# Kernel optimization log

Hardware: AMD Instinct MI355X
Metric: run time of the kernel (lower is better)

## Reference

```python
import jax, jax.numpy as jnp
import numpy as np

N_NODES = 10000
N_EDGES = 160000
BN_EPS = 1e-5


def _sage(xx, src, dst, Wl, bl, Wr, n):
    # SAGEConv: lin_l(mean of in-neighbors) + lin_r(x)
    s = jax.ops.segment_sum(xx[src], dst, num_segments=n)
    cnt = jax.ops.segment_sum(jnp.ones((src.shape[0], 1), xx.dtype), dst, num_segments=n)
    mean = s / jnp.maximum(cnt, 1.0)
    return mean @ Wl + bl + xx @ Wr


def _gin(xx, src, dst, W1, b1, W2, b2, n):
    # GINConv (eps=0): MLP(x + sum of neighbors), MLP = Lin-ReLU-Lin-ReLU
    agg = xx + jax.ops.segment_sum(xx[src], dst, num_segments=n)
    h = jax.nn.relu(agg @ W1 + b1)
    return jax.nn.relu(h @ W2 + b2)


def _gat(xx, s2, d2, W, a_s, a_d, b, heads, ch, n):
    # GATConv with self-loops already appended in (s2, d2)
    h = (xx @ W).reshape(n, heads, ch)          # [N,H,C]
    al_s = (h * a_s).sum(-1)                     # [N,H]
    al_d = (h * a_d).sum(-1)                     # [N,H]
    e = jax.nn.leaky_relu(al_s[s2] + al_d[d2], negative_slope=0.2)  # [E',H]
    m = jax.ops.segment_max(e, d2, num_segments=n)
    ex = jnp.exp(e - m[d2])
    den = jax.ops.segment_sum(ex, d2, num_segments=n)
    coef = ex / den[d2]                          # segment softmax over dst
    out = jax.ops.segment_sum(h[s2] * coef[:, :, None], d2, num_segments=n)
    return out.reshape(n, heads * ch) + b


def reference(x, edge_index, train_edge_id,
              Wp1, bp1, Wp2, bp2, Wp3, bp3,
              sage1_Wl, sage1_bl, sage1_Wr, sage2_Wl, sage2_bl, sage2_Wr,
              gin1_W1, gin1_b1, gin1_W2, gin1_b2,
              gin2_W1, gin2_b1, gin2_W2, gin2_b2, gin_lin_W, gin_lin_b,
              gat1_W, gat1_as, gat1_ad, gat1_b,
              gat2_W, gat2_as, gat2_ad, gat2_b,
              fusion_w, lin1_W, lin1_b, lin2_W, lin2_b, fc2_W, fc2_b):
    n = x.shape[0]
    src, dst = edge_index[0], edge_index[1]
    # --- ppc: PointNet-style encoder: per-point MLP (16->64->128->256) + max pool over points ---
    pts = x[:, :, :16]                            # [N,L,16]
    h = jax.nn.relu(pts @ Wp1 + bp1)
    h = jax.nn.relu(h @ Wp2 + bp2)
    h = jax.nn.relu(h @ Wp3 + bp3)
    feat = h.max(axis=1)                          # [N,256]
    # --- SAGE branch ---
    hs = jax.nn.relu(_sage(feat, src, dst, sage1_Wl, sage1_bl, sage1_Wr, n))
    out_sage = _sage(hs, src, dst, sage2_Wl, sage2_bl, sage2_Wr, n)
    # --- GIN branch ---
    hg = jax.nn.relu(_gin(feat, src, dst, gin1_W1, gin1_b1, gin1_W2, gin1_b2, n))
    hg = jax.nn.relu(_gin(hg, src, dst, gin2_W1, gin2_b1, gin2_W2, gin2_b2, n))
    out_gin = hg @ gin_lin_W + gin_lin_b
    # --- GAT branch (self-loops per PyG default) ---
    loop = jnp.arange(n)
    s2 = jnp.concatenate([src, loop])
    d2 = jnp.concatenate([dst, loop])
    ha = jax.nn.relu(_gat(feat, s2, d2, gat1_W, gat1_as, gat1_ad, gat1_b, 8, 10, n))
    out_gat = _gat(ha, s2, d2, gat2_W, gat2_as, gat2_ad, gat2_b, 1, 512, n)
    # --- weighted fusion + batch norm (batch stats, no affine) ---
    y = fusion_w[0] * out_sage + fusion_w[1] * out_gin + fusion_w[2] * out_gat
    mu = y.mean(axis=0)
    var = y.var(axis=0)
    y = (y - mu) / jnp.sqrt(var + BN_EPS)
    # --- head ---
    y = jax.nn.relu(y @ lin1_W + lin1_b)
    y = y @ lin2_W + lin2_b
    # --- edge-pair gather + multiply for link scoring ---
    nid = edge_index[:, train_edge_id]            # [2,T]
    z = y[nid[0]] * y[nid[1]]
    return z @ fc2_W + fc2_b                      # [T,7]


def setup_inputs() -> dict:
    key = jax.random.key(0)
    ks = iter(jax.random.split(key, 64))
    def nrm(shape, s=0.02):
        return jax.random.normal(next(ks), shape, dtype=jnp.float32) * s
    inp = {}
    inp['x'] = jax.random.normal(next(ks), (N_NODES, 128, 16), dtype=jnp.float32)
    inp['edge_index'] = jax.random.randint(next(ks), (2, N_EDGES), 0, N_NODES, dtype=jnp.int32)
    inp['train_edge_id'] = jax.random.randint(next(ks), (50000,), 0, N_EDGES, dtype=jnp.int32)
    # ppc point encoder
    inp['Wp1'] = nrm((16, 64)); inp['bp1'] = nrm((64,))
    inp['Wp2'] = nrm((64, 128)); inp['bp2'] = nrm((128,))
    inp['Wp3'] = nrm((128, 256)); inp['bp3'] = nrm((256,))
    # SAGE: 256->128->512
    inp['sage1_Wl'] = nrm((256, 128)); inp['sage1_bl'] = nrm((128,)); inp['sage1_Wr'] = nrm((256, 128))
    inp['sage2_Wl'] = nrm((128, 512)); inp['sage2_bl'] = nrm((512,)); inp['sage2_Wr'] = nrm((128, 512))
    # GIN: 2 convs (256->128->128, 128->128->128) + lin 128->512
    inp['gin1_W1'] = nrm((256, 128)); inp['gin1_b1'] = nrm((128,))
    inp['gin1_W2'] = nrm((128, 128)); inp['gin1_b2'] = nrm((128,))
    inp['gin2_W1'] = nrm((128, 128)); inp['gin2_b1'] = nrm((128,))
    inp['gin2_W2'] = nrm((128, 128)); inp['gin2_b2'] = nrm((128,))
    inp['gin_lin_W'] = nrm((128, 512)); inp['gin_lin_b'] = nrm((512,))
    # GAT: layer1 256 -> 8 heads x 10 (concat=80), layer2 80 -> 512 (1 head)
    inp['gat1_W'] = nrm((256, 80)); inp['gat1_as'] = nrm((8, 10)); inp['gat1_ad'] = nrm((8, 10)); inp['gat1_b'] = nrm((80,))
    inp['gat2_W'] = nrm((80, 512)); inp['gat2_as'] = nrm((1, 512)); inp['gat2_ad'] = nrm((1, 512)); inp['gat2_b'] = nrm((512,))
    # fusion + head
    inp['fusion_w'] = jnp.ones((3,), jnp.float32)
    inp['lin1_W'] = nrm((512, 512)); inp['lin1_b'] = nrm((512,))
    inp['lin2_W'] = nrm((512, 512)); inp['lin2_b'] = nrm((512,))
    inp['fc2_W'] = nrm((512, 7)); inp['fc2_b'] = nrm((7,))
    return inp
```

## Files before the change

kernel.cpp:

```cpp
#include <hip/hip_runtime.h>
#include <math.h>

#define NN 10000
#define NE 160000
#define NT 50000

typedef unsigned short u16;
typedef unsigned int u32;
typedef __attribute__((ext_vector_type(8))) short bf16x8;
typedef __attribute__((ext_vector_type(4))) float f32x4;

__device__ __forceinline__ float bf2f(u16 u) { return __uint_as_float(((u32)u) << 16); }
__device__ __forceinline__ u16 f2bf(float f) {
    u32 x = __float_as_uint(f);
    return (u16)((x + 0x7fffu + ((x >> 16) & 1u)) >> 16);
}
__device__ __forceinline__ u32 cvtpk(float a, float b) {
    u32 r;
    asm("v_cvt_pk_bf16_f32 %0, %1, %2" : "=v"(r) : "v"(a), "v"(b));
    return r;
}
__device__ __forceinline__ float lrelu(float x) { return x > 0.f ? x : 0.2f * x; }

#define MFMA16(a, b, c) __builtin_amdgcn_mfma_f32_16x16x32_bf16((a), (b), (c), 0, 0, 0)

__global__ void k_cvt_x(const float* __restrict__ x, u32* __restrict__ xb) {
    const int total = NN * 128 * 8;
    for (int i = blockIdx.x * 256 + threadIdx.x; i < total; i += gridDim.x * 256) {
        float2 v = ((const float2*)x)[i];
        xb[i] = cvtpk(v.x, v.y);
    }
}

__global__ void k_wfrag(const float* __restrict__ W1, const float* __restrict__ W2,
                        const float* __restrict__ W3,
                        u16* __restrict__ W1f, u16* __restrict__ W2f, u16* __restrict__ W3f) {
    int i = blockIdx.x * 256 + threadIdx.x;
    if (i < 2048) {
        int e = i & 7, l = (i >> 3) & 63, nt = i >> 9;
        int k = (l >> 4) * 8 + e, c = nt * 16 + (l & 15);
        W1f[i] = (k < 16) ? f2bf(W1[k * 64 + c]) : (u16)0;
    }
    if (i < 8192) {
        int e = i & 7, l = (i >> 3) & 63, nt = (i >> 9) & 7, ks = i >> 12;
        int k = ks * 32 + (l >> 4) * 8 + e, c = nt * 16 + (l & 15);
        W2f[i] = f2bf(W2[k * 128 + c]);
    }
    if (i < 32768) {
        int e = i & 7, l = (i >> 3) & 63, nt = (i >> 9) & 15, ks = i >> 13;
        int k = ks * 32 + (l >> 4) * 8 + e, c = nt * 16 + (l & 15);
        W3f[i] = f2bf(W3[k * 256 + c]);
    }
}

__global__ void k_pack(const float* __restrict__ W, u16* __restrict__ Wf, int K, int Mt) {
    int total = (((K + 63) & ~63) >> 5) * Mt * 512;
    for (int i = blockIdx.x * 256 + threadIdx.x; i < total; i += gridDim.x * 256) {
        int e = i & 7, l = (i >> 3) & 63, mt = (i >> 9) % Mt, kk = i / (Mt << 9);
        int k = (kk << 5) + ((l >> 4) << 3) + e;
        int c = (mt << 4) + (l & 15);
        Wf[i] = (k < K) ? f2bf(W[(size_t)k * (Mt << 4) + c]) : (u16)0;
    }
}

__global__ __launch_bounds__(256) void k_pointnet_mfma(
    const u16* __restrict__ xb,
    const u16* __restrict__ W1f, const float* __restrict__ b1,
    const u16* __restrict__ W2f, const float* __restrict__ b2,
    const u16* __restrict__ W3f, const float* __restrict__ b3,
    u16* __restrict__ featb)
{
    __shared__ u16 buf[16384];

    const int node = blockIdx.x;
    const int t = threadIdx.x;
    const int w = t >> 6;
    const int l = t & 63;
    const int lr = l & 15;
    const int lg = l >> 4;

    {
        bf16x8 a0 = {0,0,0,0,0,0,0,0}, a1 = a0;
        if (lg < 2) {
            const u16* px = xb + ((size_t)node * 128 + w * 32 + lr) * 16 + lg * 8;
            a0 = *(const bf16x8*)px;
            a1 = *(const bf16x8*)(px + 256);
        }
        f32x4 acc[2][4];
        #pragma unroll
        for (int nt = 0; nt < 4; ++nt) {
            float bv = b1[nt * 16 + lr];
            f32x4 ci = {bv, bv, bv, bv};
            bf16x8 bf_ = *(const bf16x8*)(W1f + (nt * 64 + l) * 8);
            acc[0][nt] = MFMA16(a0, bf_, ci);
            acc[1][nt] = MFMA16(a1, bf_, ci);
        }
        #pragma unroll
        for (int mt = 0; mt < 2; ++mt) {
            #pragma unroll
            for (int nt = 0; nt < 4; ++nt) {
                int col = nt * 16 + lr;
                int r0 = w * 32 + mt * 16 + lg * 4;
                u32 p01 = cvtpk(fmaxf(acc[mt][nt][0], 0.f), fmaxf(acc[mt][nt][1], 0.f));
                u32 p23 = cvtpk(fmaxf(acc[mt][nt][2], 0.f), fmaxf(acc[mt][nt][3], 0.f));
                buf[((r0    ) * 64 + col) ^ (((r0    ) & 7) << 3)] = (u16)p01;
                buf[((r0 + 1) * 64 + col) ^ (((r0 + 1) & 7) << 3)] = (u16)(p01 >> 16);
                buf[((r0 + 2) * 64 + col) ^ (((r0 + 2) & 7) << 3)] = (u16)p23;
                buf[((r0 + 3) * 64 + col) ^ (((r0 + 3) & 7) << 3)] = (u16)(p23 >> 16);
            }
        }
    }

    {
        bf16x8 af[2][2];
        #pragma unroll
        for (int mt = 0; mt < 2; ++mt) {
            #pragma unroll
            for (int ks = 0; ks < 2; ++ks) {
                int row = w * 32 + mt * 16 + lr;
                int elem = row * 64 + ks * 32 + lg * 8;
                af[mt][ks] = *(const bf16x8*)&buf[elem ^ ((row & 7) << 3)];
            }
        }
        __syncthreads();

        f32x4 acc2[2][8];
        #pragma unroll
        for (int nt = 0; nt < 8; ++nt) {
            float bv = b2[nt * 16 + lr];
            f32x4 ci = {bv, bv, bv, bv};
            acc2[0][nt] = ci;
            acc2[1][nt] = ci;
        }
        #pragma unroll
        for (int ks = 0; ks < 2; ++ks) {
            #pragma unroll
            for (int nt = 0; nt < 8; ++nt) {
                bf16x8 bf_ = *(const bf16x8*)(W2f + ((ks * 8 + nt) * 64 + l) * 8);
                acc2[0][nt] = MFMA16(af[0][ks], bf_, acc2[0][nt]);
                acc2[1][nt] = MFMA16(af[1][ks], bf_, acc2[1][nt]);
            }
        }
        #pragma unroll
        for (int mt = 0; mt < 2; ++mt) {
            #pragma unroll
            for (int nt = 0; nt < 8; ++nt) {
                int col = nt * 16 + lr;
                int r0 = w * 32 + mt * 16 + lg * 4;
                u32 p01 = cvtpk(fmaxf(acc2[mt][nt][0], 0.f), fmaxf(acc2[mt][nt][1], 0.f));
                u32 p23 = cvtpk(fmaxf(acc2[mt][nt][2], 0.f), fmaxf(acc2[mt][nt][3], 0.f));
                buf[((r0    ) * 128 + col) ^ (((r0    ) & 7) << 3)] = (u16)p01;
                buf[((r0 + 1) * 128 + col) ^ (((r0 + 1) & 7) << 3)] = (u16)(p01 >> 16);
                buf[((r0 + 2) * 128 + col) ^ (((r0 + 2) & 7) << 3)] = (u16)p23;
                buf[((r0 + 3) * 128 + col) ^ (((r0 + 3) & 7) << 3)] = (u16)(p23 >> 16);
            }
        }
    }
    __syncthreads();

    {
        float pmax[4] = {0.f, 0.f, 0.f, 0.f};
        #pragma unroll
        for (int half = 0; half < 2; ++half) {
            f32x4 acc3[4][4];
            #pragma unroll
            for (int nt = 0; nt < 4; ++nt) {
                float bv = b3[w * 64 + nt * 16 + lr];
                f32x4 ci = {bv, bv, bv, bv};
                #pragma unroll
                for (int mt = 0; mt < 4; ++mt) acc3[mt][nt] = ci;
            }
            #pragma unroll
            for (int ks = 0; ks < 4; ++ks) {
                bf16x8 bf_[4];
                #pragma unroll
                for (int nt = 0; nt < 4; ++nt)
                    bf_[nt] = *(const bf16x8*)(W3f + ((ks * 16 + w * 4 + nt) * 64 + l) * 8);
                #pragma unroll
                for (int mt = 0; mt < 4; ++mt) {
                    int row = half * 64 + mt * 16 + lr;
                    int elem = row * 128 + ks * 32 + lg * 8;
                    bf16x8 af = *(const bf16x8*)&buf[elem ^ ((row & 7) << 3)];
                    #pragma unroll
                    for (int nt = 0; nt < 4; ++nt)
                        acc3[mt][nt] = MFMA16(af, bf_[nt], acc3[mt][nt]);
                }
            }
            #pragma unroll
            for (int nt = 0; nt < 4; ++nt) {
                #pragma unroll
                for (int mt = 0; mt < 4; ++mt) {
                    pmax[nt] = fmaxf(fmaxf(pmax[nt], acc3[mt][nt][0]),
                                     fmaxf(acc3[mt][nt][1],
                                           fmaxf(acc3[mt][nt][2], acc3[mt][nt][3])));
                }
            }
        }
        #pragma unroll
        for (int nt = 0; nt < 4; ++nt) {
            pmax[nt] = fmaxf(pmax[nt], __shfl_xor(pmax[nt], 16));
            pmax[nt] = fmaxf(pmax[nt], __shfl_xor(pmax[nt], 32));
        }
        if (l < 16) {
            #pragma unroll
            for (int nt = 0; nt < 4; ++nt)
                featb[(size_t)node * 256 + w * 64 + nt * 16 + l] = f2bf(pmax[nt]);
        }
    }
}

template<int CT, int DUAL, int RELU, int OUTM, int NORMA>
__global__ __launch_bounds__(256) void k_mm(
    const u16* __restrict__ A, const u16* __restrict__ A2,
    const u16* __restrict__ Bf, const u16* __restrict__ B2f,
    const float* __restrict__ bias, int K, int Mt,
    void* __restrict__ outp,
    const float* __restrict__ scale_ptr, int scale_idx,
    const float* __restrict__ mu, const float* __restrict__ inv)
{
    __shared__ u16 As[8192];
    __shared__ u16 As2[DUAL ? 8192 : 8];

    const int t = threadIdx.x;
    const int l = t & 63, lr = l & 15, lg = l >> 4;
    const int row0 = blockIdx.y << 7;
    const int ct0 = blockIdx.x * CT;
    const int m0 = (t >> 6) << 5;

    f32x4 acc[2][CT];
    #pragma unroll
    for (int nt = 0; nt < CT; ++nt) {
        float bv = bias ? bias[((ct0 + nt) << 4) + lr] : 0.f;
        f32x4 ci = {bv, bv, bv, bv};
        acc[0][nt] = ci;
        acc[1][nt] = ci;
    }

    const int KS = (K + 63) >> 6;
    for (int kblk = 0; kblk < KS; ++kblk) {
        const int k0 = kblk << 6;
        if (kblk) __syncthreads();
        #pragma unroll
        for (int j = 0; j < 4; ++j) {
            int si = t + (j << 8);
            int row = si >> 3, seg = si & 7;
            int gr = row0 + row;
            int kb = k0 + (seg << 3);
            int soff = ((row << 6) + (seg << 3)) ^ ((row & 7) << 3);
            if (NORMA) {
                u32 q0 = 0, q1 = 0, q2 = 0, q3 = 0;
                if (gr < NN) {
                    const float* Af = (const float*)A;
                    float4 f0 = *(const float4*)(Af + (size_t)gr * K + kb);
                    float4 f1 = *(const float4*)(Af + (size_t)gr * K + kb + 4);
                    q0 = cvtpk((f0.x - mu[kb+0]) * inv[kb+0], (f0.y - mu[kb+1]) * inv[kb+1]);
                    q1 = cvtpk((f0.z - mu[kb+2]) * inv[kb+2], (f0.w - mu[kb+3]) * inv[kb+3]);
                    q2 = cvtpk((f1.x - mu[kb+4]) * inv[kb+4], (f1.y - mu[kb+5]) * inv[kb+5]);
                    q3 = cvtpk((f1.z - mu[kb+6]) * inv[kb+6], (f1.w - mu[kb+7]) * inv[kb+7]);
                }
                u32* dst = (u32*)&As[soff];
                dst[0] = q0; dst[1] = q1; dst[2] = q2; dst[3] = q3;
            } else {
                bf16x8 v = {0,0,0,0,0,0,0,0};
                bf16x8 v2 = {0,0,0,0,0,0,0,0};
                if (gr < NN) {
                    if (kb + 8 <= K) {
                        v = *(const bf16x8*)(A + (size_t)gr * K + kb);
                        if (DUAL) v2 = *(const bf16x8*)(A2 + (size_t)gr * K + kb);
                    } else {
                        #pragma unroll
                        for (int e = 0; e < 8; ++e) if (kb + e < K) {
                            v[e] = (short)A[(size_t)gr * K + kb + e];
                            if (DUAL) v2[e] = (short)A2[(size_t)gr * K + kb + e];
                        }
                    }
                }
                *(bf16x8*)&As[soff] = v;
                if (DUAL) *(bf16x8*)&As2[soff] = v2;
            }
        }
        __syncthreads();
        #pragma unroll
        for (int ks = 0; ks < 2; ++ks) {
            const int kk = (k0 >> 5) + ks;
            bf16x8 bfr[CT];
            #pragma unroll
            for (int nt = 0; nt < CT; ++nt)
                bfr[nt] = *(const bf16x8*)(Bf + (((size_t)kk * Mt + ct0 + nt) << 9) + (l << 3));
            #pragma unroll
            for (int mt = 0; mt < 2; ++mt) {
                int row = m0 + (mt << 4) + lr;
                int soff = ((row << 6) + (ks << 5) + (lg << 3)) ^ ((row & 7) << 3);
                bf16x8 af = *(const bf16x8*)&As[soff];
                #pragma unroll
                for (int nt = 0; nt < CT; ++nt)
                    acc[mt][nt] = MFMA16(af, bfr[nt], acc[mt][nt]);
            }
            if (DUAL) {
                bf16x8 bfr2[CT];
                #pragma unroll
                for (int nt = 0; nt < CT; ++nt)
                    bfr2[nt] = *(const bf16x8*)(B2f + (((size_t)kk * Mt + ct0 + nt) << 9) + (l << 3));
                #pragma unroll
                for (int mt = 0; mt < 2; ++mt) {
                    int row = m0 + (mt << 4) + lr;
                    int soff = ((row << 6) + (ks << 5) + (lg << 3)) ^ ((row & 7) << 3);
                    bf16x8 af2 = *(const bf16x8*)&As2[soff];
                    #pragma unroll
                    for (int nt = 0; nt < CT; ++nt)
                        acc[mt][nt] = MFMA16(af2, bfr2[nt], acc[mt][nt]);
                }
            }
        }
    }

    float scale = 1.f;
    if (OUTM == 1 || OUTM == 2) scale = scale_ptr[scale_idx];
    const int M = Mt << 4;
    #pragma unroll
    for (int mt = 0; mt < 2; ++mt) {
        #pragma unroll
        for (int nt = 0; nt < CT; ++nt) {
            int col = ((ct0 + nt) << 4) + lr;
            #pragma unroll
            for (int r = 0; r < 4; ++r) {
                int grow = row0 + m0 + (mt << 4) + (lg << 2) + r;
                if (grow >= NN) continue;
                float v = acc[mt][nt][r];
                if (RELU) v = fmaxf(v, 0.f);
                size_t o = (size_t)grow * M + col;
                if (OUTM == 0) ((u16*)outp)[o] = f2bf(v);
                else if (OUTM == 1) ((float*)outp)[o] = scale * v;
                else if (OUTM == 2) ((float*)outp)[o] += scale * v;
                else ((float*)outp)[o] = v;
            }
        }
    }
}

__global__ void k_init(int* counts, float* s1, float* s2) {
    int i = blockIdx.x * 256 + threadIdx.x;
    if (i < NN) counts[i] = 0;
    if (i < 512) { s1[i] = 0.f; s2[i] = 0.f; }
}

__global__ void k_csr_count(const int* __restrict__ EI, int* counts) {
    int e = blockIdx.x * 256 + threadIdx.x;
    if (e < NE) atomicAdd(&counts[EI[NE + e]], 1);
}

__global__ __launch_bounds__(1024) void k_scan(const int* __restrict__ counts,
                                               int* offs, int* cursor) {
    __shared__ int buf[1024];
    int t = threadIdx.x;
    int carry = 0;
    for (int chunk = 0; chunk < (NN + 1023) / 1024; ++chunk) {
        int i = chunk * 1024 + t;
        int v = (i < NN) ? counts[i] : 0;
        buf[t] = v;
        __syncthreads();
        for (int o = 1; o < 1024; o <<= 1) {
            int xv = (t >= o) ? buf[t - o] : 0;
            __syncthreads();
            buf[t] += xv;
            __syncthreads();
        }
        int excl = buf[t] - v;
        if (i < NN) { offs[i] = carry + excl; cursor[i] = carry + excl; }
        carry += buf[1023];
        __syncthreads();
    }
    if (t == 0) offs[NN] = carry;
}

__global__ void k_csr_scatter(const int* __restrict__ EI, int* cursor, int* csrc) {
    int e = blockIdx.x * 256 + threadIdx.x;
    if (e < NE) {
        int d = EI[NE + e];
        int pos = atomicAdd(&cursor[d], 1);
        csrc[pos] = EI[e];
    }
}

template<int WU, int MODE>
__global__ void k_aggb(const u32* __restrict__ in, u32* __restrict__ out,
                       const int* __restrict__ offs, const int* __restrict__ srcs)
{
    int node = blockIdx.x;
    int c = threadIdx.x;
    int o0 = offs[node], o1 = offs[node + 1];
    float s0 = 0.f, s1 = 0.f;
    for (int j = o0; j < o1; ++j) {
        u32 v = in[(size_t)srcs[j] * WU + c];
        s0 += bf2f((u16)(v & 0xffff));
        s1 += bf2f((u16)(v >> 16));
    }
    if (MODE == 0) {
        int d = o1 - o0;
        float r = 1.f / (float)(d > 0 ? d : 1);
        s0 *= r; s1 *= r;
    } else {
        u32 v = in[(size_t)node * WU + c];
        s0 += bf2f((u16)(v & 0xffff));
        s1 += bf2f((u16)(v >> 16));
    }
    out[(size_t)node * WU + c] = cvtpk(s0, s1);
}

__global__ void k_gat1_al(const u16* __restrict__ h, const float* __restrict__ a_s,
                          const float* __restrict__ a_d, float* als, float* ald) {
    int idx = blockIdx.x * 64 + threadIdx.x;
    if (idx >= NN * 8) return;
    int node = idx >> 3, hh = idx & 7;
    float s = 0.f, d = 0.f;
    #pragma unroll
    for (int c = 0; c < 10; ++c) {
        float hv = bf2f(h[node * 80 + hh * 10 + c]);
        s = fmaf(hv, a_s[hh * 10 + c], s);
        d = fmaf(hv, a_d[hh * 10 + c], d);
    }
    als[idx] = s; ald[idx] = d;
}

__global__ __launch_bounds__(128) void k_gat1_attn(
    const u16* __restrict__ h, const float* __restrict__ als,
    const float* __restrict__ ald, const float* __restrict__ bias,
    const int* __restrict__ offs, const int* __restrict__ srcs,
    u16* __restrict__ ha)
{
    int node = blockIdx.x;
    int t = threadIdx.x;
    if (t >= 80) return;
    int hh = t / 10;
    int o0 = offs[node], o1 = offs[node + 1];
    float ad = ald[node * 8 + hh];
    float eself = lrelu(als[node * 8 + hh] + ad);
    float m = eself;
    for (int j = o0; j < o1; ++j)
        m = fmaxf(m, lrelu(als[srcs[j] * 8 + hh] + ad));
    float den = 0.f, num = 0.f;
    {
        float wgt = __expf(eself - m);
        den += wgt; num += wgt * bf2f(h[(size_t)node * 80 + t]);
    }
    for (int j = o0; j < o1; ++j) {
        int sc = srcs[j];
        float wgt = __expf(lrelu(als[sc * 8 + hh] + ad) - m);
        den += wgt; num += wgt * bf2f(h[(size_t)sc * 80 + t]);
    }
    ha[(size_t)node * 80 + t] = f2bf(fmaxf(num / den + bias[t], 0.f));
}

__global__ __launch_bounds__(256) void k_gat2_al(
    const u16* __restrict__ h, const float* __restrict__ a_s,
    const float* __restrict__ a_d, float* als, float* ald)
{
    __shared__ float rs[256], rd[256];
    int node = blockIdx.x, t = threadIdx.x;
    float h0 = bf2f(h[(size_t)node * 512 + t]);
    float h1 = bf2f(h[(size_t)node * 512 + 256 + t]);
    rs[t] = h0 * a_s[t] + h1 * a_s[256 + t];
    rd[t] = h0 * a_d[t] + h1 * a_d[256 + t];
    __syncthreads();
    for (int o = 128; o > 0; o >>= 1) {
        if (t < o) { rs[t] += rs[t + o]; rd[t] += rd[t + o]; }
        __syncthreads();
    }
    if (t == 0) { als[node] = rs[0]; ald[node] = rd[0]; }
}

__global__ __launch_bounds__(256) void k_gat2_attn(
    const u16* __restrict__ h, const float* __restrict__ als,
    const float* __restrict__ ald, const float* __restrict__ bias,
    const int* __restrict__ offs, const int* __restrict__ srcs,
    const float* __restrict__ fusion_w, float* __restrict__ Y)
{
    int node = blockIdx.x;
    int t = threadIdx.x;
    float w2 = fusion_w[2];
    int o0 = offs[node], o1 = offs[node + 1];
    float ad = ald[node];
    float eself = lrelu(als[node] + ad);
    float m = eself;
    for (int j = o0; j < o1; ++j) m = fmaxf(m, lrelu(als[srcs[j]] + ad));
    float den = 0.f, n0 = 0.f, n1 = 0.f;
    {
        float wgt = __expf(eself - m);
        den += wgt;
        n0 += wgt * bf2f(h[(size_t)node * 512 + t]);
        n1 += wgt * bf2f(h[(size_t)node * 512 + 256 + t]);
    }
    for (int j = o0; j < o1; ++j) {
        int sc = srcs[j];
        float wgt = __expf(lrelu(als[sc] + ad) - m);
        den += wgt;
        n0 += wgt * bf2f(h[(size_t)sc * 512 + t]);
        n1 += wgt * bf2f(h[(size_t)sc * 512 + 256 + t]);
    }
    Y[(size_t)node * 512 + t]       += w2 * (n0 / den + bias[t]);
    Y[(size_t)node * 512 + 256 + t] += w2 * (n1 / den + bias[256 + t]);
}

__global__ __launch_bounds__(256) void k_bn_stats(const float* __restrict__ Y,
                                                  float* ssum, float* ssq) {
    int t = threadIdx.x;
    int b = blockIdx.x;
    int r0 = b * 40, r1 = r0 + 40;
    if (r1 > NN) r1 = NN;
    float s0 = 0, s1 = 0, q0 = 0, q1 = 0;
    for (int r = r0; r < r1; ++r) {
        float v0 = Y[(size_t)r * 512 + t];
        float v1 = Y[(size_t)r * 512 + 256 + t];
        s0 += v0; q0 += v0 * v0; s1 += v1; q1 += v1 * v1;
    }
    atomicAdd(&ssum[t], s0); atomicAdd(&ssum[256 + t], s1);
    atomicAdd(&ssq[t], q0);  atomicAdd(&ssq[256 + t], q1);
}

__global__ void k_bn_final(const float* ssum, const float* ssq, float* mu, float* inv) {
    int c = blockIdx.x * 256 + threadIdx.x;
    if (c < 512) {
        float m = ssum[c] / (float)NN;
        float v = ssq[c] / (float)NN - m * m;
        mu[c] = m;
        inv[c] = rsqrtf(v + 1e-5f);
    }
}

__global__ __launch_bounds__(256) void k_final(
    const float* __restrict__ y2, const int* __restrict__ EI,
    const int* __restrict__ tid, const float* __restrict__ fcW,
    const float* __restrict__ fcb, float* __restrict__ out)
{
    int pair = blockIdx.x * 4 + (threadIdx.x >> 6);
    int lane = threadIdx.x & 63;
    if (pair >= NT) return;
    int eid = tid[pair];
    int a = EI[eid], b = EI[NE + eid];
    float acc[7] = {};
    for (int c = lane; c < 512; c += 64) {
        float v = y2[(size_t)a * 512 + c] * y2[(size_t)b * 512 + c];
        #pragma unroll
        for (int j = 0; j < 7; ++j) acc[j] = fmaf(v, fcW[c * 7 + j], acc[j]);
    }
    for (int o = 32; o > 0; o >>= 1) {
        #pragma unroll
        for (int j = 0; j < 7; ++j) acc[j] += __shfl_down(acc[j], o);
    }
    if (lane == 0) {
        #pragma unroll
        for (int j = 0; j < 7; ++j) out[(size_t)pair * 7 + j] = acc[j] + fcb[j];
    }
}

extern "C" void kernel_launch(void* const* d_in, const int* in_sizes, int n_in,
                              void* d_out, int out_size, void* d_ws, size_t ws_size,
                              hipStream_t stream)
{
    (void)in_sizes; (void)n_in; (void)out_size; (void)ws_size;
    const float* x        = (const float*)d_in[0];
    const int*   EI       = (const int*)d_in[1];
    const int*   tid      = (const int*)d_in[2];
    const float* Wp1      = (const float*)d_in[3];
    const float* bp1      = (const float*)d_in[4];
    const float* Wp2      = (const float*)d_in[5];
    const float* bp2      = (const float*)d_in[6];
    const float* Wp3      = (const float*)d_in[7];
    const float* bp3      = (const float*)d_in[8];
    const float* sage1_Wl = (const float*)d_in[9];
    const float* sage1_bl = (const float*)d_in[10];
    const float* sage1_Wr = (const float*)d_in[11];
    const float* sage2_Wl = (const float*)d_in[12];
    const float* sage2_bl = (const float*)d_in[13];
    const float* sage2_Wr = (const float*)d_in[14];
    const float* gin1_W1  = (const float*)d_in[15];
    const float* gin1_b1  = (const float*)d_in[16];
    const float* gin1_W2  = (const float*)d_in[17];
    const float* gin1_b2  = (const float*)d_in[18];
    const float* gin2_W1  = (const float*)d_in[19];
    const float* gin2_b1  = (const float*)d_in[20];
    const float* gin2_W2  = (const float*)d_in[21];
    const float* gin2_b2  = (const float*)d_in[22];
    const float* gin_lin_W= (const float*)d_in[23];
    const float* gin_lin_b= (const float*)d_in[24];
    const float* gat1_W   = (const float*)d_in[25];
    const float* gat1_as  = (const float*)d_in[26];
    const float* gat1_ad  = (const float*)d_in[27];
    const float* gat1_b   = (const float*)d_in[28];
    const float* gat2_W   = (const float*)d_in[29];
    const float* gat2_as  = (const float*)d_in[30];
    const float* gat2_ad  = (const float*)d_in[31];
    const float* gat2_b   = (const float*)d_in[32];
    const float* fusion_w = (const float*)d_in[33];
    const float* lin1_W   = (const float*)d_in[34];
    const float* lin1_b   = (const float*)d_in[35];
    const float* lin2_W   = (const float*)d_in[36];
    const float* lin2_b   = (const float*)d_in[37];
    const float* fc2_W    = (const float*)d_in[38];
    const float* fc2_b    = (const float*)d_in[39];

    char* base = (char*)d_ws;
    u16* xb    = (u16*)base;
    u16* mean1 = (u16*)base;
    u16* agg1  = (u16*)(base + 5120000);
    u16* h2b   = (u16*)base;
    u16* y1b   = (u16*)(base + 20480000);
    float* y2  = (float*)base;
    size_t off = 40960000;
    u16* featb = (u16*)(base + off); off += 5120000;
    u16* hsb   = (u16*)(base + off); off += 2560000;
    u16* mean2 = (u16*)(base + off); off += 2560000;
    u16* g1    = (u16*)(base + off); off += 2560000;
    u16* g2    = (u16*)(base + off); off += 2560000;
    u16* hgat  = (u16*)(base + off); off += 1600000;
    u16* hab   = (u16*)(base + off); off += 1600000;
    float* Y   = (float*)(base + off); off += 20480000;
    float* als1 = (float*)(base + off); off += 320000;
    float* ald1 = (float*)(base + off); off += 320000;
    float* als2 = (float*)(base + off); off += 40000;
    float* ald2 = (float*)(base + off); off += 40000;
    float* ssum = (float*)(base + off); off += 2048;
    float* ssq  = (float*)(base + off); off += 2048;
    float* mu   = (float*)(base + off); off += 2048;
    float* inv  = (float*)(base + off); off += 2048;
    int* counts = (int*)(base + off); off += 40000;
    int* offs   = (int*)(base + off); off += 40016;
    int* cursor = (int*)(base + off); off += 40000;
    int* csrc   = (int*)(base + off); off += 640000;
    u16* W1f    = (u16*)(base + off); off += 4096;
    u16* W2f    = (u16*)(base + off); off += 16384;
    u16* W3f    = (u16*)(base + off); off += 65536;
    u16* s1lf   = (u16*)(base + off); off += 65536;
    u16* s1rf   = (u16*)(base + off); off += 65536;
    u16* g1w1f  = (u16*)(base + off); off += 65536;
    u16* g1w2f  = (u16*)(base + off); off += 32768;
    u16* ga1f   = (u16*)(base + off); off += 40960;
    u16* s2lf   = (u16*)(base + off); off += 131072;
    u16* s2rf   = (u16*)(base + off); off += 131072;
    u16* g2w1f  = (u16*)(base + off); off += 32768;
    u16* g2w2f  = (u16*)(base + off); off += 32768;
    u16* glinf  = (u16*)(base + off); off += 131072;
    u16* ga2f   = (u16*)(base + off); off += 131072;
    u16* l1f    = (u16*)(base + off); off += 524288;
    u16* l2f    = (u16*)(base + off); off += 524288;

    k_init<<<40, 256, 0, stream>>>(counts, ssum, ssq);
    k_cvt_x<<<2048, 256, 0, stream>>>(x, (u32*)xb);
    k_wfrag<<<128, 256, 0, stream>>>(Wp1, Wp2, Wp3, W1f, W2f, W3f);
    k_pack<<<256, 256, 0, stream>>>(sage1_Wl, s1lf, 256, 8);
    k_pack<<<256, 256, 0, stream>>>(sage1_Wr, s1rf, 256, 8);
    k_pack<<<256, 256, 0, stream>>>(gin1_W1,  g1w1f, 256, 8);
    k_pack<<<256, 256, 0, stream>>>(gin1_W2,  g1w2f, 128, 8);
    k_pack<<<256, 256, 0, stream>>>(gat1_W,   ga1f, 256, 5);
    k_pack<<<256, 256, 0, stream>>>(sage2_Wl, s2lf, 128, 32);
    k_pack<<<256, 256, 0, stream>>>(sage2_Wr, s2rf, 128, 32);
    k_pack<<<256, 256, 0, stream>>>(gin2_W1,  g2w1f, 128, 8);
    k_pack<<<256, 256, 0, stream>>>(gin2_W2,  g2w2f, 128, 8);
    k_pack<<<256, 256, 0, stream>>>(gin_lin_W, glinf, 128, 32);
    k_pack<<<256, 256, 0, stream>>>(gat2_W,   ga2f, 80, 32);
    k_pack<<<256, 256, 0, stream>>>(lin1_W,   l1f, 512, 32);
    k_pack<<<256, 256, 0, stream>>>(lin2_W,   l2f, 512, 32);

    k_pointnet_mfma<<<NN, 256, 0, stream>>>(xb, W1f, bp1, W2f, bp2, W3f, bp3, featb);
    k_csr_count<<<(NE + 255) / 256, 256, 0, stream>>>(EI, counts);
    k_scan<<<1, 1024, 0, stream>>>(counts, offs, cursor);
    k_csr_scatter<<<(NE + 255) / 256, 256, 0, stream>>>(EI, cursor, csrc);

    dim3 gN128(4, 79), gN80(5, 79), gWide(4, 79);

    k_aggb<128, 0><<<NN, 128, 0, stream>>>((const u32*)featb, (u32*)mean1, offs, csrc);
    k_aggb<128, 1><<<NN, 128, 0, stream>>>((const u32*)featb, (u32*)agg1, offs, csrc);

    k_mm<2,1,1,0,0><<<gN128, 256, 0, stream>>>(mean1, featb, s1lf, s1rf, sage1_bl,
                                               256, 8, hsb, nullptr, 0, nullptr, nullptr);
    k_mm<2,0,1,0,0><<<gN128, 256, 0, stream>>>(agg1, nullptr, g1w1f, nullptr, gin1_b1,
                                               256, 8, g1, nullptr, 0, nullptr, nullptr);
    k_mm<2,0,1,0,0><<<gN128, 256, 0, stream>>>(g1, nullptr, g1w2f, nullptr, gin1_b2,
                                               128, 8, g2, nullptr, 0, nullptr, nullptr);
    k_mm<1,0,0,0,0><<<gN80, 256, 0, stream>>>(featb, nullptr, ga1f, nullptr, nullptr,
                                              256, 5, hgat, nullptr, 0, nullptr, nullptr);
    k_gat1_al<<<1250, 64, 0, stream>>>(hgat, gat1_as, gat1_ad, als1, ald1);
    k_gat1_attn<<<NN, 128, 0, stream>>>(hgat, als1, ald1, gat1_b, offs, csrc, hab);

    k_aggb<64, 0><<<NN, 64, 0, stream>>>((const u32*)hsb, (u32*)mean2, offs, csrc);
    k_mm<8,1,0,1,0><<<gWide, 256, 0, stream>>>(mean2, hsb, s2lf, s2rf, sage2_bl,
                                               128, 32, Y, fusion_w, 0, nullptr, nullptr);
    k_aggb<64, 1><<<NN, 64, 0, stream>>>((const u32*)g2, (u32*)g1, offs, csrc);
    k_mm<2,0,1,0,0><<<gN128, 256, 0, stream>>>(g1, nullptr, g2w1f, nullptr, gin2_b1,
                                               128, 8, g2, nullptr, 0, nullptr, nullptr);
    k_mm<2,0,1,0,0><<<gN128, 256, 0, stream>>>(g2, nullptr, g2w2f, nullptr, gin2_b2,
                                               128, 8, g1, nullptr, 0, nullptr, nullptr);
    k_mm<8,0,0,2,0><<<gWide, 256, 0, stream>>>(g1, nullptr, glinf, nullptr, gin_lin_b,
                                               128, 32, Y, fusion_w, 1, nullptr, nullptr);
    k_mm<8,0,0,0,0><<<gWide, 256, 0, stream>>>(hab, nullptr, ga2f, nullptr, nullptr,
                                               80, 32, h2b, nullptr, 0, nullptr, nullptr);
    k_gat2_al<<<NN, 256, 0, stream>>>(h2b, gat2_as, gat2_ad, als2, ald2);
    k_gat2_attn<<<NN, 256, 0, stream>>>(h2b, als2, ald2, gat2_b, offs, csrc, fusion_w, Y);

    k_bn_stats<<<250, 256, 0, stream>>>(Y, ssum, ssq);
    k_bn_final<<<2, 256, 0, stream>>>(ssum, ssq, mu, inv);
    k_mm<8,0,1,0,1><<<gWide, 256, 0, stream>>>((const u16*)Y, nullptr, l1f, nullptr, lin1_b,
                                               512, 32, y1b, nullptr, 0, mu, inv);
    k_mm<8,0,0,3,0><<<gWide, 256, 0, stream>>>(y1b, nullptr, l2f, nullptr, lin2_b,
                                               512, 32, y2, nullptr, 0, nullptr, nullptr);

    k_final<<<(NT + 3) / 4, 256, 0, stream>>>(y2, EI, tid, fc2_W, fc2_b, (float*)d_out);
}
```

Baseline: 616.0 us.

## Fuse x conversion into PointNet, fuse GIN MLPs, split GAT softmax, parallelize aggregation

The fp32-to-bf16 conversion of x moves into the PointNet kernel, removing a separate pass over the input. Each GIN layer's two linears run in one kernel, with the hidden activation kept in shared memory instead of a global round-trip. GAT attention is split into a coefficient kernel that computes the per-node softmax with wave shuffles and a gather kernel where several edge slices accumulate in parallel. The aggregation kernels now use 256 threads, with edge slices reduced through shared memory. This raises parallelism for low-degree nodes but adds launches, coefficient buffers and block syncs.

```diff
diff --git a/kernel.cpp b/kernel.cpp
--- a/kernel.cpp
+++ b/kernel.cpp
@@ -23,14 +23,6 @@
 __device__ __forceinline__ float lrelu(float x) { return x > 0.f ? x : 0.2f * x; }
 
 #define MFMA16(a, b, c) __builtin_amdgcn_mfma_f32_16x16x32_bf16((a), (b), (c), 0, 0, 0)
-
-__global__ void k_cvt_x(const float* __restrict__ x, u32* __restrict__ xb) {
-    const int total = NN * 128 * 8;
-    for (int i = blockIdx.x * 256 + threadIdx.x; i < total; i += gridDim.x * 256) {
-        float2 v = ((const float2*)x)[i];
-        xb[i] = cvtpk(v.x, v.y);
-    }
-}
 
 __global__ void k_wfrag(const float* __restrict__ W1, const float* __restrict__ W2,
                         const float* __restrict__ W3,
@@ -64,7 +56,7 @@
 }
 
 __global__ __launch_bounds__(256) void k_pointnet_mfma(
-    const u16* __restrict__ xb,
+    const float* __restrict__ x,
     const u16* __restrict__ W1f, const float* __restrict__ b1,
     const u16* __restrict__ W2f, const float* __restrict__ b2,
     const u16* __restrict__ W3f, const float* __restrict__ b3,
@@ -80,11 +72,19 @@
     const int lg = l >> 4;
 
     {
-        bf16x8 a0 = {0,0,0,0,0,0,0,0}, a1 = a0;
+        union { u32 q[4]; bf16x8 v; } ua0, ua1;
+        ua0.q[0] = ua0.q[1] = ua0.q[2] = ua0.q[3] = 0;
+        ua1 = ua0;
         if (lg < 2) {
-            const u16* px = xb + ((size_t)node * 128 + w * 32 + lr) * 16 + lg * 8;
-            a0 = *(const bf16x8*)px;
-            a1 = *(const bf16x8*)(px + 256);
+            const float* px = x + ((size_t)node * 128 + w * 32 + lr) * 16 + lg * 8;
+            float4 f0 = *(const float4*)px;
+            float4 f1 = *(const float4*)(px + 4);
+            ua0.q[0] = cvtpk(f0.x, f0.y); ua0.q[1] = cvtpk(f0.z, f0.w);
+            ua0.q[2] = cvtpk(f1.x, f1.y); ua0.q[3] = cvtpk(f1.z, f1.w);
+            float4 g0 = *(const float4*)(px + 256);
+            float4 g1 = *(const float4*)(px + 260);
+            ua1.q[0] = cvtpk(g0.x, g0.y); ua1.q[1] = cvtpk(g0.z, g0.w);
+            ua1.q[2] = cvtpk(g1.x, g1.y); ua1.q[3] = cvtpk(g1.z, g1.w);
         }
         f32x4 acc[2][4];
         #pragma unroll
@@ -92,8 +92,8 @@
             float bv = b1[nt * 16 + lr];
             f32x4 ci = {bv, bv, bv, bv};
             bf16x8 bf_ = *(const bf16x8*)(W1f + (nt * 64 + l) * 8);
-            acc[0][nt] = MFMA16(a0, bf_, ci);
-            acc[1][nt] = MFMA16(a1, bf_, ci);
+            acc[0][nt] = MFMA16(ua0.v, bf_, ci);
+            acc[1][nt] = MFMA16(ua1.v, bf_, ci);
         }
         #pragma unroll
         for (int mt = 0; mt < 2; ++mt) {
@@ -338,6 +338,107 @@
     }
 }
 
+__global__ __launch_bounds__(256) void k_gin(
+    const u16* __restrict__ A, const u16* __restrict__ W1f, const float* __restrict__ b1,
+    const u16* __restrict__ W2f, const float* __restrict__ b2, int K,
+    u16* __restrict__ out)
+{
+    __shared__ u16 As[8192];
+    __shared__ u16 hb[16384];
+    const int t = threadIdx.x;
+    const int l = t & 63, lr = l & 15, lg = l >> 4;
+    const int row0 = blockIdx.x << 7;
+    const int m0 = (t >> 6) << 5;
+
+    f32x4 acc[2][8];
+    #pragma unroll
+    for (int nt = 0; nt < 8; ++nt) {
+        float bv = b1[nt * 16 + lr];
+        f32x4 ci = {bv, bv, bv, bv};
+        acc[0][nt] = ci; acc[1][nt] = ci;
+    }
+    const int KS = K >> 6;
+    for (int kblk = 0; kblk < KS; ++kblk) {
+        const int k0 = kblk << 6;
+        if (kblk) __syncthreads();
+        #pragma unroll
+        for (int j = 0; j < 4; ++j) {
+            int si = t + (j << 8);
+            int row = si >> 3, seg = si & 7;
+            int gr = row0 + row;
+            int kb = k0 + (seg << 3);
+            bf16x8 v = {0,0,0,0,0,0,0,0};
+            if (gr < NN) v = *(const bf16x8*)(A + (size_t)gr * K + kb);
+            int soff = ((row << 6) + (seg << 3)) ^ ((row & 7) << 3);
+            *(bf16x8*)&As[soff] = v;
+        }
+        __syncthreads();
+        #pragma unroll
+        for (int ks = 0; ks < 2; ++ks) {
+            const int kk = (k0 >> 5) + ks;
+            #pragma unroll
+            for (int mt = 0; mt < 2; ++mt) {
+                int row = m0 + (mt << 4) + lr;
+                int soff = ((row << 6) + (ks << 5) + (lg << 3)) ^ ((row & 7) << 3);
+                bf16x8 af = *(const bf16x8*)&As[soff];
+                #pragma unroll
+                for (int nt = 0; nt < 8; ++nt) {
+                    bf16x8 bfr = *(const bf16x8*)(W1f + ((kk * 8 + nt) * 64 + l) * 8);
+                    acc[mt][nt] = MFMA16(af, bfr, acc[mt][nt]);
+                }
+            }
+        }
+    }
+    #pragma unroll
+    for (int mt = 0; mt < 2; ++mt) {
+        #pragma unroll
+        for (int nt = 0; nt < 8; ++nt) {
+            int col = nt * 16 + lr;
+            int r0 = m0 + mt * 16 + lg * 4;
+            u32 p01 = cvtpk(fmaxf(acc[mt][nt][0], 0.f), fmaxf(acc[mt][nt][1], 0.f));
+            u32 p23 = cvtpk(fmaxf(acc[mt][nt][2], 0.f), fmaxf(acc[mt][nt][3], 0.f));
+            hb[((r0    ) * 128 + col) ^ (((r0    ) & 7) << 3)] = (u16)p01;
+            hb[((r0 + 1) * 128 + col) ^ (((r0 + 1) & 7) << 3)] = (u16)(p01 >> 16);
+            hb[((r0 + 2) * 128 + col) ^ (((r0 + 2) & 7) << 3)] = (u16)p23;
+            hb[((r0 + 3) * 128 + col) ^ (((r0 + 3) & 7) << 3)] = (u16)(p23 >> 16);
+        }
+    }
+    f32x4 acc2[2][8];
+    #pragma unroll
+    for (int nt = 0; nt < 8; ++nt) {
+        float bv = b2[nt * 16 + lr];
+        f32x4 ci = {bv, bv, bv, bv};
+        acc2[0][nt] = ci; acc2[1][nt] = ci;
+    }
+    #pragma unroll
+    for (int ks = 0; ks < 4; ++ks) {
+        #pragma unroll
+        for (int mt = 0; mt < 2; ++mt) {
+            int row = m0 + (mt << 4) + lr;
+            int elem = row * 128 + ks * 32 + lg * 8;
+            bf16x8 af = *(const bf16x8*)&hb[elem ^ ((row & 7) << 3)];
+            #pragma unroll
+            for (int nt = 0; nt < 8; ++nt) {
+                bf16x8 bfr = *(const bf16x8*)(W2f + ((ks * 8 + nt) * 64 + l) * 8);
+                acc2[mt][nt] = MFMA16(af, bfr, acc2[mt][nt]);
+            }
+        }
+    }
+    #pragma unroll
+    for (int mt = 0; mt < 2; ++mt) {
+        #pragma unroll
+        for (int nt = 0; nt < 8; ++nt) {
+            int col = nt * 16 + lr;
+            #pragma unroll
+            for (int r = 0; r < 4; ++r) {
+                int grow = row0 + m0 + mt * 16 + (lg << 2) + r;
+                if (grow >= NN) continue;
+                out[(size_t)grow * 128 + col] = f2bf(fmaxf(acc2[mt][nt][r], 0.f));
+            }
+        }
+    }
+}
+
 __global__ void k_init(int* counts, float* s1, float* s2) {
     int i = blockIdx.x * 256 + threadIdx.x;
     if (i < NN) counts[i] = 0;
@@ -383,28 +484,38 @@
 }
 
 template<int WU, int MODE>
-__global__ void k_aggb(const u32* __restrict__ in, u32* __restrict__ out,
-                       const int* __restrict__ offs, const int* __restrict__ srcs)
-{
+__global__ __launch_bounds__(256) void k_aggb(
+    const u32* __restrict__ in, u32* __restrict__ out,
+    const int* __restrict__ offs, const int* __restrict__ srcs)
+{
+    const int NSL = 256 / WU;
     int node = blockIdx.x;
-    int c = threadIdx.x;
+    int t = threadIdx.x;
+    int sl = t / WU, c = t % WU;
+    __shared__ float ps0[256], ps1[256];
     int o0 = offs[node], o1 = offs[node + 1];
     float s0 = 0.f, s1 = 0.f;
-    for (int j = o0; j < o1; ++j) {
+    for (int j = o0 + sl; j < o1; j += NSL) {
         u32 v = in[(size_t)srcs[j] * WU + c];
         s0 += bf2f((u16)(v & 0xffff));
         s1 += bf2f((u16)(v >> 16));
     }
-    if (MODE == 0) {
-        int d = o1 - o0;
-        float r = 1.f / (float)(d > 0 ? d : 1);
-        s0 *= r; s1 *= r;
-    } else {
-        u32 v = in[(size_t)node * WU + c];
-        s0 += bf2f((u16)(v & 0xffff));
-        s1 += bf2f((u16)(v >> 16));
-    }
-    out[(size_t)node * WU + c] = cvtpk(s0, s1);
+    ps0[t] = s0; ps1[t] = s1;
+    __syncthreads();
+    if (sl == 0) {
+        #pragma unroll
+        for (int s = 1; s < NSL; ++s) { s0 += ps0[s * WU + c]; s1 += ps1[s * WU + c]; }
+        if (MODE == 0) {
+            int d = o1 - o0;
+            float r = 1.f / (float)(d > 0 ? d : 1);
+            s0 *= r; s1 *= r;
+        } else {
+            u32 v = in[(size_t)node * WU + c];
+            s0 += bf2f((u16)(v & 0xffff));
+            s1 += bf2f((u16)(v >> 16));
+        }
+        out[(size_t)node * WU + c] = cvtpk(s0, s1);
+    }
 }
 
 __global__ void k_gat1_al(const u16* __restrict__ h, const float* __restrict__ a_s,
@@ -422,35 +533,6 @@
     als[idx] = s; ald[idx] = d;
 }
 
-__global__ __launch_bounds__(128) void k_gat1_attn(
-    const u16* __restrict__ h, const float* __restrict__ als,
-    const float* __restrict__ ald, const float* __restrict__ bias,
-    const int* __restrict__ offs, const int* __restrict__ srcs,
-    u16* __restrict__ ha)
-{
-    int node = blockIdx.x;
-    int t = threadIdx.x;
-    if (t >= 80) return;
-    int hh = t / 10;
-    int o0 = offs[node], o1 = offs[node + 1];
-    float ad = ald[node * 8 + hh];
-    float eself = lrelu(als[node * 8 + hh] + ad);
-    float m = eself;
-    for (int j = o0; j < o1; ++j)
-        m = fmaxf(m, lrelu(als[srcs[j] * 8 + hh] + ad));
-    float den = 0.f, num = 0.f;
-    {
-        float wgt = __expf(eself - m);
-        den += wgt; num += wgt * bf2f(h[(size_t)node * 80 + t]);
-    }
-    for (int j = o0; j < o1; ++j) {
-        int sc = srcs[j];
-        float wgt = __expf(lrelu(als[sc * 8 + hh] + ad) - m);
-        den += wgt; num += wgt * bf2f(h[(size_t)sc * 80 + t]);
-    }
-    ha[(size_t)node * 80 + t] = f2bf(fmaxf(num / den + bias[t], 0.f));
-}
-
 __global__ __launch_bounds__(256) void k_gat2_al(
     const u16* __restrict__ h, const float* __restrict__ a_s,
     const float* __restrict__ a_d, float* als, float* ald)
@@ -469,36 +551,111 @@
     if (t == 0) { als[node] = rs[0]; ald[node] = rd[0]; }
 }
 
-__global__ __launch_bounds__(256) void k_gat2_attn(
-    const u16* __restrict__ h, const float* __restrict__ als,
-    const float* __restrict__ ald, const float* __restrict__ bias,
+template<int H>
+__global__ __launch_bounds__(64) void k_gat_coef(
+    const float* __restrict__ als, const float* __restrict__ ald,
+    const int* __restrict__ offs, const int* __restrict__ srcs,
+    float* __restrict__ coef, float* __restrict__ coef_self)
+{
+    int node = blockIdx.x;
+    int l = threadIdx.x;
+    int o0 = offs[node], o1 = offs[node + 1];
+    if (H == 8) {
+        int head = l & 7, eslot = l >> 3;
+        float ad = ald[node * 8 + head];
+        float eself = lrelu(als[node * 8 + head] + ad);
+        float m = eself;
+        for (int j = o0 + eslot; j < o1; j += 8)
+            m = fmaxf(m, lrelu(als[srcs[j] * 8 + head] + ad));
+        m = fmaxf(m, __shfl_xor(m, 8));
+        m = fmaxf(m, __shfl_xor(m, 16));
+        m = fmaxf(m, __shfl_xor(m, 32));
+        float den = (eslot == 0) ? __expf(eself - m) : 0.f;
+        for (int j = o0 + eslot; j < o1; j += 8)
+            den += __expf(lrelu(als[srcs[j] * 8 + head] + ad) - m);
+        den += __shfl_xor(den, 8);
+        den += __shfl_xor(den, 16);
+        den += __shfl_xor(den, 32);
+        float rden = 1.f / den;
+        for (int j = o0 + eslot; j < o1; j += 8)
+            coef[(size_t)j * 8 + head] = __expf(lrelu(als[srcs[j] * 8 + head] + ad) - m) * rden;
+        if (eslot == 0) coef_self[node * 8 + head] = __expf(eself - m) * rden;
+    } else {
+        float ad = ald[node];
+        float eself = lrelu(als[node] + ad);
+        float m = eself;
+        for (int j = o0 + l; j < o1; j += 64)
+            m = fmaxf(m, lrelu(als[srcs[j]] + ad));
+        #pragma unroll
+        for (int o = 1; o < 64; o <<= 1) m = fmaxf(m, __shfl_xor(m, o));
+        float den = (l == 0) ? __expf(eself - m) : 0.f;
+        for (int j = o0 + l; j < o1; j += 64)
+            den += __expf(lrelu(als[srcs[j]] + ad) - m);
+        #pragma unroll
+        for (int o = 1; o < 64; o <<= 1) den += __shfl_xor(den, o);
+        float rden = 1.f / den;
+        for (int j = o0 + l; j < o1; j += 64)
+            coef[j] = __expf(lrelu(als[srcs[j]] + ad) - m) * rden;
+        if (l == 0) coef_self[node] = __expf(eself - m) * rden;
+    }
+}
+
+__global__ __launch_bounds__(256) void k_gat1_gather(
+    const u16* __restrict__ h, const float* __restrict__ coef,
+    const float* __restrict__ coef_self, const float* __restrict__ bias,
+    const int* __restrict__ offs, const int* __restrict__ srcs,
+    u16* __restrict__ ha)
+{
+    int node = blockIdx.x;
+    int t = threadIdx.x;
+    int sl = t / 80, c = t - sl * 80;
+    __shared__ float part[3][80];
+    int o0 = offs[node], o1 = offs[node + 1];
+    if (sl < 3) {
+        int head = c / 10;
+        float s = 0.f;
+        for (int j = o0 + sl; j < o1; j += 3)
+            s += coef[(size_t)j * 8 + head] * bf2f(h[(size_t)srcs[j] * 80 + c]);
+        if (sl == 0) s += coef_self[node * 8 + head] * bf2f(h[(size_t)node * 80 + c]);
+        part[sl][c] = s;
+    }
+    __syncthreads();
+    if (t < 80) {
+        float s = part[0][t] + part[1][t] + part[2][t];
+        ha[(size_t)node * 80 + t] = f2bf(fmaxf(s + bias[t], 0.f));
+    }
+}
+
+__global__ __launch_bounds__(512) void k_gat2_gather(
+    const u16* __restrict__ h, const float* __restrict__ coef,
+    const float* __restrict__ coef_self, const float* __restrict__ bias,
     const int* __restrict__ offs, const int* __restrict__ srcs,
     const float* __restrict__ fusion_w, float* __restrict__ Y)
 {
     int node = blockIdx.x;
     int t = threadIdx.x;
-    float w2 = fusion_w[2];
+    int sl = t >> 8, c = t & 255;
+    __shared__ float p0[2][256], p1[2][256];
     int o0 = offs[node], o1 = offs[node + 1];
-    float ad = ald[node];
-    float eself = lrelu(als[node] + ad);
-    float m = eself;
-    for (int j = o0; j < o1; ++j) m = fmaxf(m, lrelu(als[srcs[j]] + ad));
-    float den = 0.f, n0 = 0.f, n1 = 0.f;
-    {
-        float wgt = __expf(eself - m);
-        den += wgt;
-        n0 += wgt * bf2f(h[(size_t)node * 512 + t]);
-        n1 += wgt * bf2f(h[(size_t)node * 512 + 256 + t]);
-    }
-    for (int j = o0; j < o1; ++j) {
-        int sc = srcs[j];
-        float wgt = __expf(lrelu(als[sc] + ad) - m);
-        den += wgt;
-        n0 += wgt * bf2f(h[(size_t)sc * 512 + t]);
-        n1 += wgt * bf2f(h[(size_t)sc * 512 + 256 + t]);
-    }
-    Y[(size_t)node * 512 + t]       += w2 * (n0 / den + bias[t]);
-    Y[(size_t)node * 512 + 256 + t] += w2 * (n1 / den + bias[256 + t]);
+    float s0 = 0.f, s1 = 0.f;
+    for (int j = o0 + sl; j < o1; j += 2) {
+        float wgt = coef[j];
+        const u16* hr = h + (size_t)srcs[j] * 512;
+        s0 += wgt * bf2f(hr[c]);
+        s1 += wgt * bf2f(hr[c + 256]);
+    }
+    if (sl == 0) {
+        float wgt = coef_self[node];
+        s0 += wgt * bf2f(h[(size_t)node * 512 + c]);
+        s1 += wgt * bf2f(h[(size_t)node * 512 + 256 + c]);
+    }
+    p0[sl][c] = s0; p1[sl][c] = s1;
+    __syncthreads();
+    if (t < 256) {
+        float w2 = fusion_w[2];
+        Y[(size_t)node * 512 + t]       += w2 * (p0[0][t] + p0[1][t] + bias[t]);
+        Y[(size_t)node * 512 + 256 + t] += w2 * (p1[0][t] + p1[1][t] + bias[256 + t]);
+    }
 }
 
 __global__ __launch_bounds__(256) void k_bn_stats(const float* __restrict__ Y,
@@ -600,10 +757,13 @@
     const float* fc2_b    = (const float*)d_in[39];
 
     char* base = (char*)d_ws;
-    u16* xb    = (u16*)base;
     u16* mean1 = (u16*)base;
     u16* agg1  = (u16*)(base + 5120000);
     u16* h2b   = (u16*)base;
+    float* coef1 = (float*)(base + 10240000);
+    float* cself1= (float*)(base + 15360000);
+    float* coef2 = (float*)(base + 15680000);
+    float* cself2= (float*)(base + 16320000);
     u16* y1b   = (u16*)(base + 20480000);
     float* y2  = (float*)base;
     size_t off = 40960000;
@@ -645,7 +805,6 @@
     u16* l2f    = (u16*)(base + off); off += 524288;
 
     k_init<<<40, 256, 0, stream>>>(counts, ssum, ssq);
-    k_cvt_x<<<2048, 256, 0, stream>>>(x, (u32*)xb);
     k_wfrag<<<128, 256, 0, stream>>>(Wp1, Wp2, Wp3, W1f, W2f, W3f);
     k_pack<<<256, 256, 0, stream>>>(sage1_Wl, s1lf, 256, 8);
     k_pack<<<256, 256, 0, stream>>>(sage1_Wr, s1rf, 256, 8);
@@ -661,41 +820,37 @@
     k_pack<<<256, 256, 0, stream>>>(lin1_W,   l1f, 512, 32);
     k_pack<<<256, 256, 0, stream>>>(lin2_W,   l2f, 512, 32);
 
-    k_pointnet_mfma<<<NN, 256, 0, stream>>>(xb, W1f, bp1, W2f, bp2, W3f, bp3, featb);
+    k_pointnet_mfma<<<NN, 256, 0, stream>>>(x, W1f, bp1, W2f, bp2, W3f, bp3, featb);
     k_csr_count<<<(NE + 255) / 256, 256, 0, stream>>>(EI, counts);
     k_scan<<<1, 1024, 0, stream>>>(counts, offs, cursor);
     k_csr_scatter<<<(NE + 255) / 256, 256, 0, stream>>>(EI, cursor, csrc);
 
     dim3 gN128(4, 79), gN80(5, 79), gWide(4, 79);
 
-    k_aggb<128, 0><<<NN, 128, 0, stream>>>((const u32*)featb, (u32*)mean1, offs, csrc);
-    k_aggb<128, 1><<<NN, 128, 0, stream>>>((const u32*)featb, (u32*)agg1, offs, csrc);
+    k_aggb<128, 0><<<NN, 256, 0, stream>>>((const u32*)featb, (u32*)mean1, offs, csrc);
+    k_aggb<128, 1><<<NN, 256, 0, stream>>>((const u32*)featb, (u32*)agg1, offs, csrc);
 
     k_mm<2,1,1,0,0><<<gN128, 256, 0, stream>>>(mean1, featb, s1lf, s1rf, sage1_bl,
                                                256, 8, hsb, nullptr, 0, nullptr, nullptr);
-    k_mm<2,0,1,0,0><<<gN128, 256, 0, stream>>>(agg1, nullptr, g1w1f, nullptr, gin1_b1,
-                                               256, 8, g1, nullptr, 0, nullptr, nullptr);
-    k_mm<2,0,1,0,0><<<gN128, 256, 0, stream>>>(g1, nullptr, g1w2f, nullptr, gin1_b2,
-                                               128, 8, g2, nullptr, 0, nullptr, nullptr);
+    k_gin<<<79, 256, 0, stream>>>(agg1, g1w1f, gin1_b1, g1w2f, gin1_b2, 256, g1);
     k_mm<1,0,0,0,0><<<gN80, 256, 0, stream>>>(featb, nullptr, ga1f, nullptr, nullptr,
                                               256, 5, hgat, nullptr, 0, nullptr, nullptr);
     k_gat1_al<<<1250, 64, 0, stream>>>(hgat, gat1_as, gat1_ad, als1, ald1);
-    k_gat1_attn<<<NN, 128, 0, stream>>>(hgat, als1, ald1, gat1_b, offs, csrc, hab);
-
-    k_aggb<64, 0><<<NN, 64, 0, stream>>>((const u32*)hsb, (u32*)mean2, offs, csrc);
+    k_gat_coef<8><<<NN, 64, 0, stream>>>(als1, ald1, offs, csrc, coef1, cself1);
+    k_gat1_gather<<<NN, 256, 0, stream>>>(hgat, coef1, cself1, gat1_b, offs, csrc, hab);
+
+    k_aggb<64, 0><<<NN, 256, 0, stream>>>((const u32*)hsb, (u32*)mean2, offs, csrc);
     k_mm<8,1,0,1,0><<<gWide, 256, 0, stream>>>(mean2, hsb, s2lf, s2rf, sage2_bl,
                                                128, 32, Y, fusion_w, 0, nullptr, nullptr);
-    k_aggb<64, 1><<<NN, 64, 0, stream>>>((const u32*)g2, (u32*)g1, offs, csrc);
-    k_mm<2,0,1,0,0><<<gN128, 256, 0, stream>>>(g1, nullptr, g2w1f, nullptr, gin2_b1,
-                                               128, 8, g2, nullptr, 0, nullptr, nullptr);
-    k_mm<2,0,1,0,0><<<gN128, 256, 0, stream>>>(g2, nullptr, g2w2f, nullptr, gin2_b2,
-                                               128, 8, g1, nullptr, 0, nullptr, nullptr);
+    k_aggb<64, 1><<<NN, 256, 0, stream>>>((const u32*)g1, (u32*)g2, offs, csrc);
+    k_gin<<<79, 256, 0, stream>>>(g2, g2w1f, gin2_b1, g2w2f, gin2_b2, 128, g1);
     k_mm<8,0,0,2,0><<<gWide, 256, 0, stream>>>(g1, nullptr, glinf, nullptr, gin_lin_b,
                                                128, 32, Y, fusion_w, 1, nullptr, nullptr);
     k_mm<8,0,0,0,0><<<gWide, 256, 0, stream>>>(hab, nullptr, ga2f, nullptr, nullptr,
                                                80, 32, h2b, nullptr, 0, nullptr, nullptr);
     k_gat2_al<<<NN, 256, 0, stream>>>(h2b, gat2_as, gat2_ad, als2, ald2);
-    k_gat2_attn<<<NN, 256, 0, stream>>>(h2b, als2, ald2, gat2_b, offs, csrc, fusion_w, Y);
+    k_gat_coef<1><<<NN, 64, 0, stream>>>(als2, ald2, offs, csrc, coef2, cself2);
+    k_gat2_gather<<<NN, 512, 0, stream>>>(h2b, coef2, cself2, gat2_b, offs, csrc, fusion_w, Y);
 
     k_bn_stats<<<250, 256, 0, stream>>>(Y, ssum, ssq);
     k_bn_final<<<2, 256, 0, stream>>>(ssum, ssq, mu, inv);
```

Result: slower. 638.1 us (+3.6%).
